# Kernel optimization log

Measured on AMD Instinct MI355X. Metric: run time of the kernel, lower is better.

The kernel has to match this reference:

```python
import jax, jax.numpy as jnp
import numpy as np

K_UP = 5
UP = 2
KS = 3
C_IN = 256


def pixel_shuffle(x, r):
    N, C, H, W = x.shape
    x = x.reshape(N, C // (r * r), r, r, H, W)
    return x.transpose(0, 1, 4, 2, 5, 3).reshape(N, C // (r * r), H * r, W * r)


def conv2d(x, w, b, pad):
    y = jax.lax.conv_general_dilated(
        x, w, window_strides=(1, 1), padding=[(pad, pad), (pad, pad)],
        dimension_numbers=('NCHW', 'OIHW', 'NCHW'))
    return y + b[None, :, None, None]


def setup_inputs() -> dict:
    key = jax.random.key(0)
    ks = jax.random.split(key, 7)
    C = C_IN
    Cd = C // 2
    Ce = UP * UP * K_UP * K_UP  # 100
    x = jax.random.normal(ks[0], (4, C, 64, 64), dtype=jnp.float32)
    # kaiming-normal-ish inits, biases small uniform (torch default)
    w_down = jax.random.normal(ks[1], (Cd, C, 1, 1), dtype=jnp.float32) * np.sqrt(2.0 / C)
    b_down = jax.random.uniform(ks[2], (Cd,), dtype=jnp.float32, minval=-0.05, maxval=0.05)
    w_enc = jax.random.normal(ks[3], (Ce, Cd, KS, KS), dtype=jnp.float32) * np.sqrt(2.0 / (Cd * KS * KS))
    b_enc = jax.random.uniform(ks[4], (Ce,), dtype=jnp.float32, minval=-0.05, maxval=0.05)
    w_out = jax.random.normal(ks[5], (C, C, 1, 1), dtype=jnp.float32) * np.sqrt(2.0 / C)
    b_out = jax.random.uniform(ks[6], (C,), dtype=jnp.float32, minval=-0.05, maxval=0.05)
    return {"x": x, "w_down": w_down, "b_down": b_down, "w_enc": w_enc,
            "b_enc": b_enc, "w_out": w_out, "b_out": b_out}


def reference(x, w_down, b_down, w_enc, b_enc, w_out, b_out):
    N, C, H, W = x.shape
    k2 = K_UP * K_UP  # 25
    u2 = UP * UP      # 4
    # kernel prediction branch
    kt = conv2d(x, w_down, b_down, 0)
    kt = conv2d(kt, w_enc, b_enc, KS // 2)
    kt = pixel_shuffle(kt, UP)              # (N, 25, H*UP, W*UP)
    kt = jax.nn.softmax(kt, axis=1)
    # unfold(2,UP,UP).unfold(3,UP,UP) -> (N,25,H,W,UP,UP) -> (N,H,W,25,UP*UP)
    kt = kt.reshape(N, k2, H, UP, W, UP).transpose(0, 2, 4, 1, 3, 5)
    kt = kt.reshape(N, H, W, k2, u2)
    # feature patches: pad then gather k_up x k_up window per pixel
    pad = K_UP // 2
    xp = jnp.pad(x, ((0, 0), (0, 0), (pad, pad), (pad, pad)))
    patches = jnp.stack(
        [xp[:, :, i:i + H, j:j + W] for i in range(K_UP) for j in range(K_UP)],
        axis=-1)                            # (N, C, H, W, 25)
    # per-pixel weighted sum: (N,H,W,C,25) @ (N,H,W,25,u2)
    out = jnp.einsum('nchwk,nhwkp->nchwp', patches, kt)  # (N,C,H,W,u2)
    out = out.transpose(0, 1, 4, 2, 3).reshape(N, C * u2, H, W)
    out = pixel_shuffle(out, UP)            # (N, C, H*UP, W*UP)
    return conv2d(out, w_out, b_out, 0)
```

## Files before the change

kernel.cpp:

```cpp
#include <hip/hip_runtime.h>
#include <hip/hip_bf16.h>


#define NB    4
#define NPIX  4096

typedef short s16x8 __attribute__((ext_vector_type(8)));
typedef float f32x4 __attribute__((ext_vector_type(4)));

#define MFMA16(a, b, c) __builtin_amdgcn_mfma_f32_16x16x32_bf16((a), (b), (c), 0, 0, 0)

__device__ __forceinline__ ushort f2b(float f) {
    __hip_bfloat16 h = __float2bfloat16(f);
    return *(ushort*)&h;
}
__device__ __forceinline__ float b2f(ushort u) {
    unsigned v = ((unsigned)u) << 16;
    return *(float*)&v;
}

__global__ __launch_bounds__(256) void prep_kernel(
    const float* __restrict__ wd, const float* __restrict__ wo,
    const float* __restrict__ we,
    ushort* __restrict__ wcomb, ushort* __restrict__ wrb)
{
    int idx = blockIdx.x * 256 + threadIdx.x;
    if (idx < 98304) {
        float v = (idx < 32768) ? wd[idx] : wo[idx - 32768];
        wcomb[idx] = f2b(v);
    } else if (idx < 227328) {
        int i = idx - 98304;
        int co = i / 1152, k = i - co * 1152;
        int tap = k >> 7, c = k & 127;
        float v = (co < 100) ? we[(co * 128 + c) * 9 + tap] : 0.0f;
        wrb[i] = f2b(v);
    }
}

__global__ __launch_bounds__(256, 2) void dual_gemm_kernel(
    const float*  __restrict__ X,
    const ushort* __restrict__ Wcomb,
    const float*  __restrict__ b_down,
    ushort* __restrict__ T1t,
    ushort* __restrict__ XOt)
{
    __shared__ __attribute__((aligned(16))) ushort xs[32][264];
    const int n = blockIdx.y, p0 = blockIdx.x * 32;
    const int tid = threadIdx.x, lane = tid & 63, wid = tid >> 6;
    const int l15 = lane & 15, l4 = lane >> 4;

    {
        const int pix4  = tid & 7;
        const int cpair = tid >> 3;
        const float* base = X + (size_t)n * 256 * NPIX + p0 + pix4 * 4;
        #pragma unroll
        for (int pp = 0; pp < 4; pp++) {
            int c = pp * 64 + cpair * 2;
            float4 va = *(const float4*)&base[(size_t)c * NPIX];
            float4 vb = *(const float4*)&base[(size_t)(c + 1) * NPIX];
            float va_[4] = {va.x, va.y, va.z, va.w};
            float vb_[4] = {vb.x, vb.y, vb.z, vb.w};
            #pragma unroll
            for (int j = 0; j < 4; j++) {
                ushort2 w;
                w.x = f2b(va_[j]);
                w.y = f2b(vb_[j]);
                *(ushort2*)&xs[pix4 * 4 + j][c] = w;
            }
        }
    }
    __syncthreads();

    const int wp = wid & 1;
    const int wc = wid >> 1;
    const int crow = wc * 192;

    f32x4 acc[12] = {};
    #pragma unroll 2
    for (int ks = 0; ks < 8; ks++) {
        int k0 = ks * 32 + l4 * 8;
        s16x8 a = *(const s16x8*)&xs[wp * 16 + l15][k0];
        #pragma unroll
        for (int cf = 0; cf < 12; cf++) {
            s16x8 b = *(const s16x8*)&Wcomb[(size_t)(crow + cf * 16 + l15) * 256 + k0];
            acc[cf] = MFMA16(a, b, acc[cf]);
        }
    }

    #pragma unroll
    for (int cf = 0; cf < 12; cf++) {
        int cbase = crow + cf * 16;
        int c = cbase + l15;
        if (cbase < 128) {
            float bb = b_down[c];
            #pragma unroll
            for (int r = 0; r < 4; r++) {
                int pix = p0 + wp * 16 + l4 * 4 + r;
                T1t[(size_t)(n * NPIX + pix) * 128 + c] = f2b(acc[cf][r] + bb);
            }
        } else {
            int c2 = c - 128;
            #pragma unroll
            for (int r = 0; r < 4; r++) {
                int pix = p0 + wp * 16 + l4 * 4 + r;
                XOt[(size_t)(n * NPIX + pix) * 256 + c2] = f2b(acc[cf][r]);
            }
        }
    }
}

__global__ __launch_bounds__(256, 3) void conv_sm_kernel(
    const ushort* __restrict__ T1t,
    const ushort* __restrict__ Wr,
    const float*  __restrict__ Benc,
    float* __restrict__ SMg)
{
    __shared__ __attribute__((aligned(16))) ushort hs[100][136];
    __shared__ float eld[64][101];

    const int n = blockIdx.y, tile = blockIdx.x;
    const int h0 = (tile >> 3) * 8, w0 = (tile & 7) * 8;
    const int tid = threadIdx.x, lane = tid & 63, wid = tid >> 6;
    const int l15 = lane & 15, l4 = lane >> 4;

    for (int u = tid; u < 1600; u += 256) {
        int hp = u >> 4, ch = u & 15;
        int r = hp / 10, s = hp - r * 10;
        int gh = h0 - 1 + r, gw = w0 - 1 + s;
        s16x8 v = {};
        if ((unsigned)gh < 64u && (unsigned)gw < 64u)
            v = *(const s16x8*)&T1t[((size_t)n * NPIX + gh * 64 + gw) * 128 + ch * 8];
        *(s16x8*)&hs[hp][ch * 8] = v;
    }
    __syncthreads();

    {
        const int pl = wid * 16 + l15;
        const int ph = pl >> 3, pw = pl & 7;
        f32x4 acc[7] = {};
        for (int tap = 0; tap < 9; tap++) {
            int dy = tap / 3, dx = tap - dy * 3;
            int hp = (ph + dy) * 10 + pw + dx;
            const ushort* hrow = &hs[hp][l4 * 8];
            const ushort* wrow = &Wr[(size_t)l15 * 1152 + tap * 128 + l4 * 8];
            #pragma unroll
            for (int cb = 0; cb < 4; cb++) {
                s16x8 b = *(const s16x8*)&hrow[cb * 32];
                #pragma unroll
                for (int mf = 0; mf < 7; mf++) {
                    s16x8 a = *(const s16x8*)&wrow[(size_t)mf * 16 * 1152 + cb * 32];
                    acc[mf] = MFMA16(a, b, acc[mf]);
                }
            }
        }
        #pragma unroll
        for (int mf = 0; mf < 7; mf++) {
            #pragma unroll
            for (int r = 0; r < 4; r++) {
                int co = mf * 16 + l4 * 4 + r;
                if (co < 100) eld[pl][co] = acc[mf][r] + Benc[co];
            }
        }
    }
    __syncthreads();

    {
        int p = tid & 3, pix = tid >> 2;
        float v[25];
        float mx = -1e30f;
        #pragma unroll
        for (int k = 0; k < 25; k++) { v[k] = eld[pix][4 * k + p]; mx = fmaxf(mx, v[k]); }
        float ssum = 0.0f;
        #pragma unroll
        for (int k = 0; k < 25; k++) { v[k] = __expf(v[k] - mx); ssum += v[k]; }
        float inv = 1.0f / ssum;
        float* dst = SMg + (size_t)(n * 64 + tile) * 6400;
        #pragma unroll
        for (int k = 0; k < 25; k++)
            dst[k * 256 + tid] = v[k] * inv;
    }
}

__global__ __launch_bounds__(256, 2) void reassembly_kernel(
    const float*  __restrict__ SMg,
    const ushort* __restrict__ XOt,
    const float*  __restrict__ Bout,
    float* __restrict__ Z)
{
    __shared__ __attribute__((aligned(16))) float sml[64][100];
    __shared__ float xs[64][145];

    const int tile = blockIdx.x, oc = blockIdx.y, n = blockIdx.z;
    const int h0 = (tile >> 3) * 8, w0 = (tile & 7) * 8;
    const int tid = threadIdx.x;

    {
        const float* src = SMg + (size_t)(n * 64 + tile) * 6400;
        int pix = tid >> 2, p = tid & 3;
        #pragma unroll
        for (int j = 0; j < 25; j++)
            sml[pix][j * 4 + p] = src[j * 256 + tid];
    }

    for (int u = tid; u < 2304; u += 256) {
        int hp = u >> 4, cg = u & 15;
        int r = hp / 12, s = hp - r * 12;
        int gh = h0 - 2 + r, gw = w0 - 2 + s;
        float v0 = 0.f, v1 = 0.f, v2 = 0.f, v3 = 0.f;
        if ((unsigned)gh < 64u && (unsigned)gw < 64u) {
            ushort4 raw = *(const ushort4*)&XOt[((size_t)n * NPIX + gh * 64 + gw) * 256 + oc * 64 + cg * 4];
            v0 = b2f(raw.x); v1 = b2f(raw.y); v2 = b2f(raw.z); v3 = b2f(raw.w);
        }
        xs[cg * 4 + 0][hp] = v0;
        xs[cg * 4 + 1][hp] = v1;
        xs[cg * 4 + 2][hp] = v2;
        xs[cg * 4 + 3][hp] = v3;
    }
    __syncthreads();

    const int pw2 = tid & 3;
    const int ph  = (tid >> 2) & 7;
    const int og  = tid >> 5;
    const int pix0 = ph * 8 + pw2 * 2;

    float acc[8][8] = {};
    for (int k = 0; k < 25; k++) {
        int di = k / 5, dj = k - di * 5;
        float4 wv0 = *(const float4*)&sml[pix0][k * 4];
        float4 wv1 = *(const float4*)&sml[pix0 + 1][k * 4];
        int base = (ph + di) * 12 + pw2 * 2 + dj;
        #pragma unroll
        for (int i = 0; i < 8; i++) {
            float xv0 = xs[og * 8 + i][base];
            float xv1 = xs[og * 8 + i][base + 1];
            acc[i][0] += xv0 * wv0.x;
            acc[i][1] += xv0 * wv0.y;
            acc[i][2] += xv0 * wv0.z;
            acc[i][3] += xv0 * wv0.w;
            acc[i][4] += xv1 * wv1.x;
            acc[i][5] += xv1 * wv1.y;
            acc[i][6] += xv1 * wv1.z;
            acc[i][7] += xv1 * wv1.w;
        }
    }

    const int gh = h0 + ph;
    #pragma unroll
    for (int i = 0; i < 8; i++) {
        int o = oc * 64 + og * 8 + i;
        float bb = Bout[o];
        float4 v0 = make_float4(acc[i][0] + bb, acc[i][1] + bb, acc[i][4] + bb, acc[i][5] + bb);
        float4 v1 = make_float4(acc[i][2] + bb, acc[i][3] + bb, acc[i][6] + bb, acc[i][7] + bb);
        size_t zb = (((size_t)n * 256 + o) * 128 + 2 * gh) * 128 + 2 * w0 + 4 * pw2;
        *(float4*)&Z[zb]       = v0;
        *(float4*)&Z[zb + 128] = v1;
    }
}

extern "C" void kernel_launch(void* const* d_in, const int* in_sizes, int n_in,
                              void* d_out, int out_size, void* d_ws, size_t ws_size,
                              hipStream_t stream) {
    const float* x      = (const float*)d_in[0];
    const float* w_down = (const float*)d_in[1];
    const float* b_down = (const float*)d_in[2];
    const float* w_enc  = (const float*)d_in[3];
    const float* b_enc  = (const float*)d_in[4];
    const float* w_out  = (const float*)d_in[5];
    const float* b_out  = (const float*)d_in[6];
    float* z = (float*)d_out;

    ushort* t1T   = (ushort*)d_ws;
    ushort* xoT   = t1T + 2097152;
    ushort* wcomb = xoT + 4194304;
    ushort* wrb   = wcomb + 98304;
    float*  smg   = (float*)(wrb + 129024);

    prep_kernel<<<888, 256, 0, stream>>>(w_down, w_out, w_enc, wcomb, wrb);
    dual_gemm_kernel<<<dim3(128, NB), 256, 0, stream>>>(x, wcomb, b_down, t1T, xoT);
    conv_sm_kernel<<<dim3(64, NB), 256, 0, stream>>>(t1T, wrb, b_enc, smg);
    reassembly_kernel<<<dim3(64, 4, NB), 256, 0, stream>>>(smg, xoT, b_out, z);
}
```

Measured before the change: 174.2 us.

## Fuse encoder conv+softmax into reassembly kernel and shrink GEMM tiles

Merges the 3x3 encoder conv and softmax kernel with the reassembly kernel, so the softmax weights stay in shared memory instead of going through a global buffer. The conv and softmax are now recomputed once per output-channel group (4x redundant). The dual GEMM tile is halved to 16 pixels per block with an XOR-swizzled LDS layout and higher occupancy. Reassembly keeps the XO tile as bf16 in swizzled LDS and prefetches it into registers before the conv, trading more registers and redundant MFMA work for one fewer launch and less global traffic.

```diff
diff --git a/kernel.cpp b/kernel.cpp
--- a/kernel.cpp
+++ b/kernel.cpp
@@ -37,88 +37,85 @@
     }
 }
 
-__global__ __launch_bounds__(256, 2) void dual_gemm_kernel(
+__global__ __launch_bounds__(256, 4) void dual_gemm_kernel(
     const float*  __restrict__ X,
     const ushort* __restrict__ Wcomb,
     const float*  __restrict__ b_down,
     ushort* __restrict__ T1t,
     ushort* __restrict__ XOt)
 {
-    __shared__ __attribute__((aligned(16))) ushort xs[32][264];
-    const int n = blockIdx.y, p0 = blockIdx.x * 32;
+    __shared__ __attribute__((aligned(16))) ushort xs[16 * 264];
+    const int n = blockIdx.y, p0 = blockIdx.x * 16;
     const int tid = threadIdx.x, lane = tid & 63, wid = tid >> 6;
     const int l15 = lane & 15, l4 = lane >> 4;
 
     {
-        const int pix4  = tid & 7;
-        const int cpair = tid >> 3;
-        const float* base = X + (size_t)n * 256 * NPIX + p0 + pix4 * 4;
-        #pragma unroll
-        for (int pp = 0; pp < 4; pp++) {
-            int c = pp * 64 + cpair * 2;
-            float4 va = *(const float4*)&base[(size_t)c * NPIX];
-            float4 vb = *(const float4*)&base[(size_t)(c + 1) * NPIX];
-            float va_[4] = {va.x, va.y, va.z, va.w};
-            float vb_[4] = {vb.x, vb.y, vb.z, vb.w};
+        const int pq = tid & 3;
+        const float* src = X + (size_t)n * 256 * NPIX + p0 + pq * 4;
+        #pragma unroll
+        for (int pass = 0; pass < 4; pass++) {
+            int c = pass * 64 + (tid >> 2);
+            float4 v = *(const float4*)&src[(size_t)c * NPIX];
+            float vv[4] = {v.x, v.y, v.z, v.w};
             #pragma unroll
             for (int j = 0; j < 4; j++) {
-                ushort2 w;
-                w.x = f2b(va_[j]);
-                w.y = f2b(vb_[j]);
-                *(ushort2*)&xs[pix4 * 4 + j][c] = w;
-            }
-        }
-    }
-    __syncthreads();
-
-    const int wp = wid & 1;
-    const int wc = wid >> 1;
-    const int crow = wc * 192;
-
-    f32x4 acc[12] = {};
-    #pragma unroll 2
+                int px = pq * 4 + j;
+                xs[px * 264 + (c ^ ((px & 7) << 3))] = f2b(vv[j]);
+            }
+        }
+    }
+    __syncthreads();
+
+    const int crow = wid * 96;
+    f32x4 acc[6] = {};
+    #pragma unroll
     for (int ks = 0; ks < 8; ks++) {
         int k0 = ks * 32 + l4 * 8;
-        s16x8 a = *(const s16x8*)&xs[wp * 16 + l15][k0];
-        #pragma unroll
-        for (int cf = 0; cf < 12; cf++) {
+        s16x8 a = *(const s16x8*)&xs[l15 * 264 + (k0 ^ ((l15 & 7) << 3))];
+        #pragma unroll
+        for (int cf = 0; cf < 6; cf++) {
             s16x8 b = *(const s16x8*)&Wcomb[(size_t)(crow + cf * 16 + l15) * 256 + k0];
             acc[cf] = MFMA16(a, b, acc[cf]);
         }
     }
 
     #pragma unroll
-    for (int cf = 0; cf < 12; cf++) {
+    for (int cf = 0; cf < 6; cf++) {
         int cbase = crow + cf * 16;
         int c = cbase + l15;
         if (cbase < 128) {
             float bb = b_down[c];
             #pragma unroll
             for (int r = 0; r < 4; r++) {
-                int pix = p0 + wp * 16 + l4 * 4 + r;
+                int pix = p0 + l4 * 4 + r;
                 T1t[(size_t)(n * NPIX + pix) * 128 + c] = f2b(acc[cf][r] + bb);
             }
         } else {
             int c2 = c - 128;
             #pragma unroll
             for (int r = 0; r < 4; r++) {
-                int pix = p0 + wp * 16 + l4 * 4 + r;
+                int pix = p0 + l4 * 4 + r;
                 XOt[(size_t)(n * NPIX + pix) * 256 + c2] = f2b(acc[cf][r]);
             }
         }
     }
 }
 
-__global__ __launch_bounds__(256, 3) void conv_sm_kernel(
+__global__ __launch_bounds__(256, 3) void carafe3_kernel(
     const ushort* __restrict__ T1t,
     const ushort* __restrict__ Wr,
     const float*  __restrict__ Benc,
-    float* __restrict__ SMg)
+    const ushort* __restrict__ XOt,
+    const float*  __restrict__ Bout,
+    float* __restrict__ Z)
 {
-    __shared__ __attribute__((aligned(16))) ushort hs[100][136];
-    __shared__ float eld[64][101];
-
-    const int n = blockIdx.y, tile = blockIdx.x;
+    __shared__ __attribute__((aligned(16))) char smem[27200 + 25856];
+    ushort* hs  = (ushort*)smem;
+    float*  sml = (float*)smem;
+    float*  eld = (float*)(smem + 27200);
+    ushort* xsu = (ushort*)(smem + 27200);
+
+    const int tile = blockIdx.x, oc = blockIdx.y, n = blockIdx.z;
     const int h0 = (tile >> 3) * 8, w0 = (tile & 7) * 8;
     const int tid = threadIdx.x, lane = tid & 63, wid = tid >> 6;
     const int l15 = lane & 15, l4 = lane >> 4;
@@ -130,18 +127,30 @@
         s16x8 v = {};
         if ((unsigned)gh < 64u && (unsigned)gw < 64u)
             v = *(const s16x8*)&T1t[((size_t)n * NPIX + gh * 64 + gw) * 128 + ch * 8];
-        *(s16x8*)&hs[hp][ch * 8] = v;
+        *(s16x8*)&hs[hp * 136 + ch * 8] = v;
+    }
+    ushort4 xoreg[9];
+    #pragma unroll
+    for (int t = 0; t < 9; t++) {
+        int u = tid + t * 256;
+        int hp = u >> 4, cg = u & 15;
+        int r = hp / 12, s = hp - r * 12;
+        int gh = h0 - 2 + r, gw = w0 - 2 + s;
+        ushort4 v = make_ushort4(0, 0, 0, 0);
+        if ((unsigned)gh < 64u && (unsigned)gw < 64u)
+            v = *(const ushort4*)&XOt[((size_t)n * NPIX + gh * 64 + gw) * 256 + oc * 64 + cg * 4];
+        xoreg[t] = v;
     }
     __syncthreads();
 
     {
         const int pl = wid * 16 + l15;
-        const int ph = pl >> 3, pw = pl & 7;
-        f32x4 acc[7] = {};
+        const int ph_ = pl >> 3, pw_ = pl & 7;
+        f32x4 cacc[7] = {};
         for (int tap = 0; tap < 9; tap++) {
             int dy = tap / 3, dx = tap - dy * 3;
-            int hp = (ph + dy) * 10 + pw + dx;
-            const ushort* hrow = &hs[hp][l4 * 8];
+            int hp = (ph_ + dy) * 10 + pw_ + dx;
+            const ushort* hrow = &hs[hp * 136 + l4 * 8];
             const ushort* wrow = &Wr[(size_t)l15 * 1152 + tap * 128 + l4 * 8];
             #pragma unroll
             for (int cb = 0; cb < 4; cb++) {
@@ -149,7 +158,7 @@
                 #pragma unroll
                 for (int mf = 0; mf < 7; mf++) {
                     s16x8 a = *(const s16x8*)&wrow[(size_t)mf * 16 * 1152 + cb * 32];
-                    acc[mf] = MFMA16(a, b, acc[mf]);
+                    cacc[mf] = MFMA16(a, b, cacc[mf]);
                 }
             }
         }
@@ -158,7 +167,7 @@
             #pragma unroll
             for (int r = 0; r < 4; r++) {
                 int co = mf * 16 + l4 * 4 + r;
-                if (co < 100) eld[pl][co] = acc[mf][r] + Benc[co];
+                if (co < 100) eld[pl * 101 + co] = cacc[mf][r] + Benc[co];
             }
         }
     }
@@ -166,55 +175,29 @@
 
     {
         int p = tid & 3, pix = tid >> 2;
+        int s = (pix >> 1) & 7;
         float v[25];
         float mx = -1e30f;
         #pragma unroll
-        for (int k = 0; k < 25; k++) { v[k] = eld[pix][4 * k + p]; mx = fmaxf(mx, v[k]); }
+        for (int k = 0; k < 25; k++) { v[k] = eld[pix * 101 + 4 * k + p]; mx = fmaxf(mx, v[k]); }
         float ssum = 0.0f;
         #pragma unroll
         for (int k = 0; k < 25; k++) { v[k] = __expf(v[k] - mx); ssum += v[k]; }
         float inv = 1.0f / ssum;
-        float* dst = SMg + (size_t)(n * 64 + tile) * 6400;
-        #pragma unroll
-        for (int k = 0; k < 25; k++)
-            dst[k * 256 + tid] = v[k] * inv;
-    }
-}
-
-__global__ __launch_bounds__(256, 2) void reassembly_kernel(
-    const float*  __restrict__ SMg,
-    const ushort* __restrict__ XOt,
-    const float*  __restrict__ Bout,
-    float* __restrict__ Z)
-{
-    __shared__ __attribute__((aligned(16))) float sml[64][100];
-    __shared__ float xs[64][145];
-
-    const int tile = blockIdx.x, oc = blockIdx.y, n = blockIdx.z;
-    const int h0 = (tile >> 3) * 8, w0 = (tile & 7) * 8;
-    const int tid = threadIdx.x;
-
-    {
-        const float* src = SMg + (size_t)(n * 64 + tile) * 6400;
-        int pix = tid >> 2, p = tid & 3;
-        #pragma unroll
-        for (int j = 0; j < 25; j++)
-            sml[pix][j * 4 + p] = src[j * 256 + tid];
-    }
-
-    for (int u = tid; u < 2304; u += 256) {
+        #pragma unroll
+        for (int k = 0; k < 25; k++) {
+            int blk = k + s; if (blk >= 25) blk -= 25;
+            sml[pix * 100 + blk * 4 + p] = v[k] * inv;
+        }
+    }
+    __syncthreads();
+
+    #pragma unroll
+    for (int t = 0; t < 9; t++) {
+        int u = tid + t * 256;
         int hp = u >> 4, cg = u & 15;
-        int r = hp / 12, s = hp - r * 12;
-        int gh = h0 - 2 + r, gw = w0 - 2 + s;
-        float v0 = 0.f, v1 = 0.f, v2 = 0.f, v3 = 0.f;
-        if ((unsigned)gh < 64u && (unsigned)gw < 64u) {
-            ushort4 raw = *(const ushort4*)&XOt[((size_t)n * NPIX + gh * 64 + gw) * 256 + oc * 64 + cg * 4];
-            v0 = b2f(raw.x); v1 = b2f(raw.y); v2 = b2f(raw.z); v3 = b2f(raw.w);
-        }
-        xs[cg * 4 + 0][hp] = v0;
-        xs[cg * 4 + 1][hp] = v1;
-        xs[cg * 4 + 2][hp] = v2;
-        xs[cg * 4 + 3][hp] = v3;
+        int blk = (cg >> 1) ^ (hp & 7);
+        *(ushort4*)&xsu[hp * 72 + blk * 8 + (cg & 1) * 4] = xoreg[t];
     }
     __syncthreads();
 
@@ -222,25 +205,30 @@
     const int ph  = (tid >> 2) & 7;
     const int og  = tid >> 5;
     const int pix0 = ph * 8 + pw2 * 2;
+    const int s0 = (pix0 >> 1) & 7;
 
     float acc[8][8] = {};
     for (int k = 0; k < 25; k++) {
         int di = k / 5, dj = k - di * 5;
-        float4 wv0 = *(const float4*)&sml[pix0][k * 4];
-        float4 wv1 = *(const float4*)&sml[pix0 + 1][k * 4];
-        int base = (ph + di) * 12 + pw2 * 2 + dj;
+        int blk = k + s0; if (blk >= 25) blk -= 25;
+        f32x4 wv0 = *(const f32x4*)&sml[pix0 * 100 + blk * 4];
+        f32x4 wv1 = *(const f32x4*)&sml[(pix0 + 1) * 100 + blk * 4];
+        int b0 = (ph + di) * 12 + pw2 * 2 + dj;
+        int b1 = b0 + 1;
+        s16x8 x0 = *(const s16x8*)&xsu[b0 * 72 + ((og ^ (b0 & 7)) << 3)];
+        s16x8 x1 = *(const s16x8*)&xsu[b1 * 72 + ((og ^ (b1 & 7)) << 3)];
         #pragma unroll
         for (int i = 0; i < 8; i++) {
-            float xv0 = xs[og * 8 + i][base];
-            float xv1 = xs[og * 8 + i][base + 1];
-            acc[i][0] += xv0 * wv0.x;
-            acc[i][1] += xv0 * wv0.y;
-            acc[i][2] += xv0 * wv0.z;
-            acc[i][3] += xv0 * wv0.w;
-            acc[i][4] += xv1 * wv1.x;
-            acc[i][5] += xv1 * wv1.y;
-            acc[i][6] += xv1 * wv1.z;
-            acc[i][7] += xv1 * wv1.w;
+            float f0 = b2f((ushort)x0[i]);
+            float f1 = b2f((ushort)x1[i]);
+            acc[i][0] += f0 * wv0[0];
+            acc[i][1] += f0 * wv0[1];
+            acc[i][2] += f0 * wv0[2];
+            acc[i][3] += f0 * wv0[3];
+            acc[i][4] += f1 * wv1[0];
+            acc[i][5] += f1 * wv1[1];
+            acc[i][6] += f1 * wv1[2];
+            acc[i][7] += f1 * wv1[3];
         }
     }
 
@@ -273,10 +261,8 @@
     ushort* xoT   = t1T + 2097152;
     ushort* wcomb = xoT + 4194304;
     ushort* wrb   = wcomb + 98304;
-    float*  smg   = (float*)(wrb + 129024);
 
     prep_kernel<<<888, 256, 0, stream>>>(w_down, w_out, w_enc, wcomb, wrb);
-    dual_gemm_kernel<<<dim3(128, NB), 256, 0, stream>>>(x, wcomb, b_down, t1T, xoT);
-    conv_sm_kernel<<<dim3(64, NB), 256, 0, stream>>>(t1T, wrb, b_enc, smg);
-    reassembly_kernel<<<dim3(64, 4, NB), 256, 0, stream>>>(smg, xoT, b_out, z);
-}
+    dual_gemm_kernel<<<dim3(256, NB), 256, 0, stream>>>(x, wcomb, b_down, t1T, xoT);
+    carafe3_kernel<<<dim3(64, 4, NB), 256, 0, stream>>>(t1T, wrb, b_enc, xoT, b_out, z);
+}
```

After: 240.0 us. 1.38x slower.
